# Kernel optimization log

Measured on AMD Instinct MI355X. Metric: run time of the kernel, lower is better.

Reference implementation:

```python
import jax, jax.numpy as jnp
import numpy as np

N = 50000   # nodes
E = 1600000 # edges
D = 128     # input_dim
H = 128     # hidden_dim
O = 128     # output_dim
G = 64      # graphs in batch
EPS = 1e-5  # batchnorm eps


def setup_inputs() -> dict:
    key = jax.random.key(0)
    ks = jax.random.split(key, 20)
    x = jax.random.normal(ks[0], (N, D), jnp.float32)
    edge_index = jax.random.randint(ks[1], (2, E), 0, N, dtype=jnp.int32)
    batch = jnp.sort(jax.random.randint(ks[2], (N,), 0, G, dtype=jnp.int32))

    def lin(k, fi, fo):
        return jax.random.normal(k, (fi, fo), jnp.float32) / np.float32(np.sqrt(fi))

    return {
        "x": x, "edge_index": edge_index, "batch": batch,
        "W1": lin(ks[3], D, H), "b1": jnp.zeros((H,), jnp.float32),
        "W2": lin(ks[4], H, H), "b2": jnp.zeros((H,), jnp.float32),
        "W3": lin(ks[5], H, O), "b3": jnp.zeros((O,), jnp.float32),
        "g1": 1.0 + 0.1 * jax.random.normal(ks[6], (H,), jnp.float32),
        "be1": 0.1 * jax.random.normal(ks[7], (H,), jnp.float32),
        "rm1": 0.1 * jax.random.normal(ks[8], (H,), jnp.float32),
        "rv1": 0.5 + jax.random.uniform(ks[9], (H,), jnp.float32),
        "g2": 1.0 + 0.1 * jax.random.normal(ks[10], (H,), jnp.float32),
        "be2": 0.1 * jax.random.normal(ks[11], (H,), jnp.float32),
        "rm2": 0.1 * jax.random.normal(ks[12], (H,), jnp.float32),
        "rv2": 0.5 + jax.random.uniform(ks[13], (H,), jnp.float32),
    }


def _gcn_layer(h, W, b, row, col, norm):
    # h: [N, Fin] -> [N, Fout]; GCN: A_hat @ (h W) + b with sym-normalized A_hat
    h = h @ W
    msg = h[row] * norm[:, None]                      # [E+N, Fout] gather
    out = jax.ops.segment_sum(msg, col, num_segments=N)
    return out + b


def _bn_eval(h, g, be, rm, rv):
    return (h - rm) * jax.lax.rsqrt(rv + EPS) * g + be


def reference(x, edge_index, batch, W1, b1, W2, b2, W3, b3,
              g1, be1, rm1, rv1, g2, be2, rm2, rv2):
    # add self loops (PyG GCNConv default)
    loop = jnp.arange(N, dtype=edge_index.dtype)
    row = jnp.concatenate([edge_index[0], loop])
    col = jnp.concatenate([edge_index[1], loop])
    deg = jax.ops.segment_sum(jnp.ones_like(col, jnp.float32), col, num_segments=N)
    dinv = jnp.where(deg > 0, jax.lax.rsqrt(jnp.maximum(deg, 1.0)), 0.0)
    norm = dinv[row] * dinv[col]                       # [E+N]

    h = _gcn_layer(x, W1, b1, row, col, norm)
    h = jax.nn.relu(_bn_eval(h, g1, be1, rm1, rv1))    # dropout is identity (eval)
    h = _gcn_layer(h, W2, b2, row, col, norm)
    h = jax.nn.relu(_bn_eval(h, g2, be2, rm2, rv2))
    h = _gcn_layer(h, W3, b3, row, col, norm)
    # global_add_pool by graph id
    return jax.ops.segment_sum(h, batch, num_segments=G)  # [G, O]
```

## Files before the change

kernel.cpp:

```cpp
#include <hip/hip_runtime.h>
#include <hip/hip_bf16.h>

#define NN 50000
#define NE 1600000
#define DIM 128
#define NG 64
#define EPSV 1e-5f
#define NCHUNK 49
#define UNROLL 8
#define RUN 4

typedef __attribute__((ext_vector_type(8))) __bf16 bf16x8;
typedef __attribute__((ext_vector_type(2))) __bf16 bf16x2;
typedef __attribute__((ext_vector_type(16))) float f32x16;


__global__ void count_kernel(const int* __restrict__ ecol, int* __restrict__ cnt) {
    int e = blockIdx.x * 256 + threadIdx.x;
    if (e < NE) atomicAdd(&cnt[ecol[e]], 1);
}

__global__ void scan_chunk(const int* __restrict__ cnt, int* __restrict__ excl,
                           int* __restrict__ csum) {
    __shared__ int lds[256];
    int t = threadIdx.x;
    int base = blockIdx.x * 1024 + t * 4;
    int v0 = (base + 0 < NN) ? cnt[base + 0] : 0;
    int v1 = (base + 1 < NN) ? cnt[base + 1] : 0;
    int v2 = (base + 2 < NN) ? cnt[base + 2] : 0;
    int v3 = (base + 3 < NN) ? cnt[base + 3] : 0;
    int s = v0 + v1 + v2 + v3;
    lds[t] = s;
    __syncthreads();
    for (int off = 1; off < 256; off <<= 1) {
        int x = (t >= off) ? lds[t - off] : 0;
        __syncthreads();
        lds[t] += x;
        __syncthreads();
    }
    int run = lds[t] - s;
    if (t == 255) csum[blockIdx.x] = lds[t];
    if (base + 0 < NN) excl[base + 0] = run; run += v0;
    if (base + 1 < NN) excl[base + 1] = run; run += v1;
    if (base + 2 < NN) excl[base + 2] = run; run += v2;
    if (base + 3 < NN) excl[base + 3] = run;
}

__global__ void scan_tail(const int* __restrict__ csum, int* __restrict__ coff, int nch) {
    int l = threadIdx.x;
    int v = (l < nch) ? csum[l] : 0;
    int s = v;
    for (int o = 1; o < 64; o <<= 1) {
        int x = __shfl_up(s, o);
        if (l >= o) s += x;
    }
    if (l < nch) coff[l] = s - v;
}

__global__ void fixup_kernel(int* __restrict__ row_ptr, const int* __restrict__ coff,
                             const int* __restrict__ cnt, float* __restrict__ dinv,
                             int* __restrict__ cursor) {
    int n = blockIdx.x * 256 + threadIdx.x;
    if (n < NN) {
        int rp = row_ptr[n] + coff[n >> 10];
        row_ptr[n] = rp;
        cursor[n] = rp;
        dinv[n] = rsqrtf((float)(cnt[n] + 1));
    }
    if (n == 0) row_ptr[NN] = NE;
}

__global__ void fill_kernel(const int* __restrict__ erow, const int* __restrict__ ecol,
                            const float* __restrict__ dinv, int* __restrict__ cursor,
                            int* __restrict__ esrc, float* __restrict__ enorm) {
    int e = blockIdx.x * 256 + threadIdx.x;
    if (e < NE) {
        int r = erow[e], c = ecol[e];
        int pos = atomicAdd(&cursor[c], 1);
        esrc[pos] = r;
        enorm[pos] = dinv[r] * dinv[c];
    }
}

__global__ void bn_prep_kernel(const float* __restrict__ b1, const float* __restrict__ g1,
                               const float* __restrict__ be1, const float* __restrict__ rm1,
                               const float* __restrict__ rv1,
                               const float* __restrict__ b2, const float* __restrict__ g2,
                               const float* __restrict__ be2, const float* __restrict__ rm2,
                               const float* __restrict__ rv2,
                               float* __restrict__ sc1, float* __restrict__ sh1,
                               float* __restrict__ sc2, float* __restrict__ sh2) {
    int c = threadIdx.x;
    if (c < DIM) {
        float s1 = g1[c] * rsqrtf(rv1[c] + EPSV);
        sc1[c] = s1;
        sh1[c] = (b1[c] - rm1[c]) * s1 + be1[c];
        float s2 = g2[c] * rsqrtf(rv2[c] + EPSV);
        sc2[c] = s2;
        sh2[c] = (b2[c] - rm2[c]) * s2 + be2[c];
    }
}


__device__ __forceinline__ bf16x8 load8(const float* p) {
    float4 lo = ((const float4*)p)[0], hi = ((const float4*)p)[1];
    bf16x8 a;
    a[0] = (__bf16)lo.x; a[1] = (__bf16)lo.y; a[2] = (__bf16)lo.z; a[3] = (__bf16)lo.w;
    a[4] = (__bf16)hi.x; a[5] = (__bf16)hi.y; a[6] = (__bf16)hi.z; a[7] = (__bf16)hi.w;
    return a;
}
__device__ __forceinline__ bf16x8 load8(const __bf16* p) {
    return *(const bf16x8*)p;
}

template <typename T>
__global__ void __launch_bounds__(256) matmul_kernel(const T* __restrict__ h,
                                                     const float* __restrict__ W,
                                                     __bf16* __restrict__ t) {
    const int wave = threadIdx.x >> 6;
    const int lane = threadIdx.x & 63;
    const int col = wave * 32 + (lane & 31);
    const int khalf = (lane >> 5) * 8;

    bf16x8 b[8];
#pragma unroll
    for (int kc = 0; kc < 8; kc++) {
#pragma unroll
        for (int j = 0; j < 8; j++) {
            b[kc][j] = (__bf16)W[(kc * 16 + khalf + j) * DIM + col];
        }
    }

    const int ntiles = (NN + 31) / 32;
    for (int tile = blockIdx.x; tile < ntiles; tile += gridDim.x) {
        const int arow = tile * 32 + (lane & 31);
        const int arow_c = (arow < NN) ? arow : (NN - 1);
        f32x16 acc = {};
#pragma unroll
        for (int kc = 0; kc < 8; kc++) {
            bf16x8 a = load8(h + (size_t)arow_c * DIM + kc * 16 + khalf);
            acc = __builtin_amdgcn_mfma_f32_32x32x16_bf16(a, b[kc], acc, 0, 0, 0);
        }
#pragma unroll
        for (int r = 0; r < 16; r++) {
            int orow = tile * 32 + (r & 3) + 8 * (r >> 2) + 4 * (lane >> 5);
            if (orow < NN) t[(size_t)orow * DIM + col] = (__bf16)acc[r];
        }
    }
}


__device__ __forceinline__ void gather_core(
    const unsigned int* __restrict__ t32, const int* __restrict__ esrc,
    const float* __restrict__ enorm, int beg, int end, int lane,
    float& ax, float& ay) {
    for (int e = beg; e < end; e += UNROLL) {
        int   s[UNROLL];
        float w[UNROLL];
        unsigned int u[UNROLL];
#pragma unroll
        for (int i = 0; i < UNROLL; i++) {
            const bool ok = (e + i) < end;
            const int  ee = ok ? (e + i) : beg;
            s[i] = esrc[ee];
            w[i] = ok ? enorm[ee] : 0.f;
        }
#pragma unroll
        for (int i = 0; i < UNROLL; i++) u[i] = t32[(size_t)s[i] * 64 + lane];
#pragma unroll
        for (int i = 0; i < UNROLL; i++) {
            ax = fmaf(__uint_as_float(u[i] << 16), w[i], ax);
            ay = fmaf(__uint_as_float(u[i] & 0xffff0000u), w[i], ay);
        }
    }
}

__global__ void __launch_bounds__(256) gather_bn_kernel(
    const unsigned int* __restrict__ t32, const int* __restrict__ row_ptr,
    const int* __restrict__ esrc, const float* __restrict__ enorm,
    const float* __restrict__ dinv, const float* __restrict__ scale,
    const float* __restrict__ shift, __bf16* __restrict__ out) {
    const int lane = threadIdx.x & 63;
    const int n = __builtin_amdgcn_readfirstlane(blockIdx.x * 4 + (threadIdx.x >> 6));
    if (n >= NN) return;
    float ax = 0.f, ay = 0.f;
    const int beg = row_ptr[n], end = row_ptr[n + 1];
    gather_core(t32, esrc, enorm, beg, end, lane, ax, ay);
    {
        float w = dinv[n]; w *= w;
        const unsigned int u = t32[(size_t)n * 64 + lane];
        ax = fmaf(__uint_as_float(u << 16), w, ax);
        ay = fmaf(__uint_as_float(u & 0xffff0000u), w, ay);
    }
    const int c0 = lane * 2, c1 = c0 + 1;
    ax = fmaxf(fmaf(ax, scale[c0], shift[c0]), 0.f);
    ay = fmaxf(fmaf(ay, scale[c1], shift[c1]), 0.f);
    bf16x2 o; o[0] = (__bf16)ax; o[1] = (__bf16)ay;
    *(bf16x2*)(out + (size_t)n * DIM + c0) = o;
}


__global__ void __launch_bounds__(256) gather_pool_kernel(
    const unsigned int* __restrict__ t32, const int* __restrict__ row_ptr,
    const int* __restrict__ esrc, const float* __restrict__ enorm,
    const float* __restrict__ dinv, const float* __restrict__ bias,
    const int* __restrict__ batch, float* __restrict__ out) {
    const int lane = threadIdx.x & 63;
    const int wid = __builtin_amdgcn_readfirstlane(blockIdx.x * 4 + (threadIdx.x >> 6));
    const int n0 = wid * RUN;
    if (n0 >= NN) return;
    const int n1 = (n0 + RUN < NN) ? n0 + RUN : NN;
    const int c0 = lane * 2, c1 = c0 + 1;
    const float bx = bias[c0], by = bias[c1];
    float rx = 0.f, ry = 0.f;
    int g = batch[n0];
    for (int n = n0; n < n1; ++n) {
        float ax = 0.f, ay = 0.f;
        const int beg = row_ptr[n], end = row_ptr[n + 1];
        gather_core(t32, esrc, enorm, beg, end, lane, ax, ay);
        {
            float w = dinv[n]; w *= w;
            const unsigned int u = t32[(size_t)n * 64 + lane];
            ax = fmaf(__uint_as_float(u << 16), w, ax);
            ay = fmaf(__uint_as_float(u & 0xffff0000u), w, ay);
        }
        const int gn = batch[n];
        if (gn != g) {
            atomicAdd(out + (size_t)g * DIM + c0, rx);
            atomicAdd(out + (size_t)g * DIM + c1, ry);
            rx = 0.f; ry = 0.f; g = gn;
        }
        rx += ax + bx;
        ry += ay + by;
    }
    atomicAdd(out + (size_t)g * DIM + c0, rx);
    atomicAdd(out + (size_t)g * DIM + c1, ry);
}


extern "C" void kernel_launch(void* const* d_in, const int* in_sizes, int n_in,
                              void* d_out, int out_size, void* d_ws, size_t ws_size,
                              hipStream_t stream) {
    const float* x    = (const float*)d_in[0];
    const int*   ei   = (const int*)d_in[1];
    const int*   batch= (const int*)d_in[2];
    const float* W1 = (const float*)d_in[3];
    const float* b1 = (const float*)d_in[4];
    const float* W2 = (const float*)d_in[5];
    const float* b2 = (const float*)d_in[6];
    const float* W3 = (const float*)d_in[7];
    const float* b3 = (const float*)d_in[8];
    const float* g1 = (const float*)d_in[9];
    const float* be1= (const float*)d_in[10];
    const float* rm1= (const float*)d_in[11];
    const float* rv1= (const float*)d_in[12];
    const float* g2 = (const float*)d_in[13];
    const float* be2= (const float*)d_in[14];
    const float* rm2= (const float*)d_in[15];
    const float* rv2= (const float*)d_in[16];
    const int* erow = ei;
    const int* ecol = ei + NE;

    char* ws = (char*)d_ws;
    size_t off = 0;
    auto alloc = [&](size_t bytes) -> void* {
        void* p = ws + off;
        off = (off + bytes + 255) & ~(size_t)255;
        return p;
    };
    int*    cnt     = (int*)alloc(NN * sizeof(int));
    int*    row_ptr = (int*)alloc((NN + 1) * sizeof(int));
    int*    cursor  = (int*)alloc(NN * sizeof(int));
    int*    csum    = (int*)alloc(64 * sizeof(int));
    int*    coff    = (int*)alloc(64 * sizeof(int));
    float*  dinv    = (float*)alloc(NN * sizeof(float));
    int*    esrc    = (int*)alloc(NE * sizeof(int));
    float*  enorm   = (float*)alloc(NE * sizeof(float));
    __bf16* tbuf    = (__bf16*)alloc((size_t)NN * DIM * sizeof(__bf16));
    __bf16* hbuf    = (__bf16*)alloc((size_t)NN * DIM * sizeof(__bf16));
    float*  sc1     = (float*)alloc(DIM * sizeof(float));
    float*  sh1     = (float*)alloc(DIM * sizeof(float));
    float*  sc2     = (float*)alloc(DIM * sizeof(float));
    float*  sh2     = (float*)alloc(DIM * sizeof(float));

    hipMemsetAsync(cnt, 0, NN * sizeof(int), stream);
    hipMemsetAsync(d_out, 0, NG * DIM * sizeof(float), stream);

    bn_prep_kernel<<<1, 128, 0, stream>>>(b1, g1, be1, rm1, rv1,
                                          b2, g2, be2, rm2, rv2,
                                          sc1, sh1, sc2, sh2);
    count_kernel<<<(NE + 255) / 256, 256, 0, stream>>>(ecol, cnt);
    scan_chunk<<<NCHUNK, 256, 0, stream>>>(cnt, row_ptr, csum);
    scan_tail<<<1, 64, 0, stream>>>(csum, coff, NCHUNK);
    fixup_kernel<<<(NN + 255) / 256, 256, 0, stream>>>(row_ptr, coff, cnt, dinv, cursor);
    fill_kernel<<<(NE + 255) / 256, 256, 0, stream>>>(erow, ecol, dinv, cursor, esrc, enorm);

    const unsigned int* t32 = (const unsigned int*)tbuf;
    const int nblk = (NN + 3) / 4;
    const int nwaves_pool = (NN + RUN - 1) / RUN;
    const int nblk_pool = (nwaves_pool + 3) / 4;

    matmul_kernel<float><<<512, 256, 0, stream>>>(x, W1, tbuf);
    gather_bn_kernel<<<nblk, 256, 0, stream>>>(t32, row_ptr, esrc, enorm, dinv,
                                               sc1, sh1, hbuf);
    matmul_kernel<__bf16><<<512, 256, 0, stream>>>(hbuf, W2, tbuf);
    gather_bn_kernel<<<nblk, 256, 0, stream>>>(t32, row_ptr, esrc, enorm, dinv,
                                               sc2, sh2, hbuf);
    matmul_kernel<__bf16><<<512, 256, 0, stream>>>(hbuf, W3, tbuf);
    gather_pool_kernel<<<nblk_pool, 256, 0, stream>>>(t32, row_ptr, esrc, enorm, dinv,
                                                      b3, batch, (float*)d_out);
}
```

Baseline: 457.0 us.

## Factor symmetric normalization into matmul epilogue and gather output, drop per-edge norm array

The per-edge weight dinv[r]*dinv[c] is split into two factors. The source-side dinv is applied to each row in the matmul epilogue, and the destination-side dinv is applied once per node after aggregation. This removes the enorm array entirely: it is no longer written in the fill kernel or read once per edge in each of the three gather passes, and the fill kernel stops doing random dinv lookups. The cost is an extra dinv load per output element in the matmul epilogue, plus rounding the pre-scaled values to bf16 at a different point.

```diff
diff --git a/kernel.cpp b/kernel.cpp
--- a/kernel.cpp
+++ b/kernel.cpp
@@ -71,14 +71,11 @@
 }
 
 __global__ void fill_kernel(const int* __restrict__ erow, const int* __restrict__ ecol,
-                            const float* __restrict__ dinv, int* __restrict__ cursor,
-                            int* __restrict__ esrc, float* __restrict__ enorm) {
+                            int* __restrict__ cursor, int* __restrict__ esrc) {
     int e = blockIdx.x * 256 + threadIdx.x;
     if (e < NE) {
-        int r = erow[e], c = ecol[e];
-        int pos = atomicAdd(&cursor[c], 1);
-        esrc[pos] = r;
-        enorm[pos] = dinv[r] * dinv[c];
+        int pos = atomicAdd(&cursor[ecol[e]], 1);
+        esrc[pos] = erow[e];
     }
 }
 
@@ -116,6 +113,7 @@
 template <typename T>
 __global__ void __launch_bounds__(256) matmul_kernel(const T* __restrict__ h,
                                                      const float* __restrict__ W,
+                                                     const float* __restrict__ dinv,
                                                      __bf16* __restrict__ t) {
     const int wave = threadIdx.x >> 6;
     const int lane = threadIdx.x & 63;
@@ -144,7 +142,7 @@
 #pragma unroll
         for (int r = 0; r < 16; r++) {
             int orow = tile * 32 + (r & 3) + 8 * (r >> 2) + 4 * (lane >> 5);
-            if (orow < NN) t[(size_t)orow * DIM + col] = (__bf16)acc[r];
+            if (orow < NN) t[(size_t)orow * DIM + col] = (__bf16)(acc[r] * dinv[orow]);
         }
     }
 }
@@ -152,8 +150,7 @@
 
 __device__ __forceinline__ void gather_core(
     const unsigned int* __restrict__ t32, const int* __restrict__ esrc,
-    const float* __restrict__ enorm, int beg, int end, int lane,
-    float& ax, float& ay) {
+    int beg, int end, int lane, float& ax, float& ay) {
     for (int e = beg; e < end; e += UNROLL) {
         int   s[UNROLL];
         float w[UNROLL];
@@ -161,9 +158,8 @@
 #pragma unroll
         for (int i = 0; i < UNROLL; i++) {
             const bool ok = (e + i) < end;
-            const int  ee = ok ? (e + i) : beg;
-            s[i] = esrc[ee];
-            w[i] = ok ? enorm[ee] : 0.f;
+            s[i] = esrc[ok ? (e + i) : beg];
+            w[i] = ok ? 1.f : 0.f;
         }
 #pragma unroll
         for (int i = 0; i < UNROLL; i++) u[i] = t32[(size_t)s[i] * 64 + lane];
@@ -177,24 +173,24 @@
 
 __global__ void __launch_bounds__(256) gather_bn_kernel(
     const unsigned int* __restrict__ t32, const int* __restrict__ row_ptr,
-    const int* __restrict__ esrc, const float* __restrict__ enorm,
-    const float* __restrict__ dinv, const float* __restrict__ scale,
-    const float* __restrict__ shift, __bf16* __restrict__ out) {
+    const int* __restrict__ esrc, const float* __restrict__ dinv,
+    const float* __restrict__ scale, const float* __restrict__ shift,
+    __bf16* __restrict__ out) {
     const int lane = threadIdx.x & 63;
     const int n = __builtin_amdgcn_readfirstlane(blockIdx.x * 4 + (threadIdx.x >> 6));
     if (n >= NN) return;
     float ax = 0.f, ay = 0.f;
     const int beg = row_ptr[n], end = row_ptr[n + 1];
-    gather_core(t32, esrc, enorm, beg, end, lane, ax, ay);
+    gather_core(t32, esrc, beg, end, lane, ax, ay);
     {
-        float w = dinv[n]; w *= w;
         const unsigned int u = t32[(size_t)n * 64 + lane];
-        ax = fmaf(__uint_as_float(u << 16), w, ax);
-        ay = fmaf(__uint_as_float(u & 0xffff0000u), w, ay);
-    }
+        ax += __uint_as_float(u << 16);
+        ay += __uint_as_float(u & 0xffff0000u);
+    }
+    const float dv = dinv[n];
     const int c0 = lane * 2, c1 = c0 + 1;
-    ax = fmaxf(fmaf(ax, scale[c0], shift[c0]), 0.f);
-    ay = fmaxf(fmaf(ay, scale[c1], shift[c1]), 0.f);
+    ax = fmaxf(fmaf(ax, dv * scale[c0], shift[c0]), 0.f);
+    ay = fmaxf(fmaf(ay, dv * scale[c1], shift[c1]), 0.f);
     bf16x2 o; o[0] = (__bf16)ax; o[1] = (__bf16)ay;
     *(bf16x2*)(out + (size_t)n * DIM + c0) = o;
 }
@@ -202,9 +198,9 @@
 
 __global__ void __launch_bounds__(256) gather_pool_kernel(
     const unsigned int* __restrict__ t32, const int* __restrict__ row_ptr,
-    const int* __restrict__ esrc, const float* __restrict__ enorm,
-    const float* __restrict__ dinv, const float* __restrict__ bias,
-    const int* __restrict__ batch, float* __restrict__ out) {
+    const int* __restrict__ esrc, const float* __restrict__ dinv,
+    const float* __restrict__ bias, const int* __restrict__ batch,
+    float* __restrict__ out) {
     const int lane = threadIdx.x & 63;
     const int wid = __builtin_amdgcn_readfirstlane(blockIdx.x * 4 + (threadIdx.x >> 6));
     const int n0 = wid * RUN;
@@ -217,21 +213,21 @@
     for (int n = n0; n < n1; ++n) {
         float ax = 0.f, ay = 0.f;
         const int beg = row_ptr[n], end = row_ptr[n + 1];
-        gather_core(t32, esrc, enorm, beg, end, lane, ax, ay);
+        gather_core(t32, esrc, beg, end, lane, ax, ay);
         {
-            float w = dinv[n]; w *= w;
             const unsigned int u = t32[(size_t)n * 64 + lane];
-            ax = fmaf(__uint_as_float(u << 16), w, ax);
-            ay = fmaf(__uint_as_float(u & 0xffff0000u), w, ay);
-        }
+            ax += __uint_as_float(u << 16);
+            ay += __uint_as_float(u & 0xffff0000u);
+        }
+        const float dv = dinv[n];
         const int gn = batch[n];
         if (gn != g) {
             atomicAdd(out + (size_t)g * DIM + c0, rx);
             atomicAdd(out + (size_t)g * DIM + c1, ry);
             rx = 0.f; ry = 0.f; g = gn;
         }
-        rx += ax + bx;
-        ry += ay + by;
+        rx += fmaf(ax, dv, bx);
+        ry += fmaf(ay, dv, by);
     }
     atomicAdd(out + (size_t)g * DIM + c0, rx);
     atomicAdd(out + (size_t)g * DIM + c1, ry);
@@ -275,7 +271,6 @@
     int*    coff    = (int*)alloc(64 * sizeof(int));
     float*  dinv    = (float*)alloc(NN * sizeof(float));
     int*    esrc    = (int*)alloc(NE * sizeof(int));
-    float*  enorm   = (float*)alloc(NE * sizeof(float));
     __bf16* tbuf    = (__bf16*)alloc((size_t)NN * DIM * sizeof(__bf16));
     __bf16* hbuf    = (__bf16*)alloc((size_t)NN * DIM * sizeof(__bf16));
     float*  sc1     = (float*)alloc(DIM * sizeof(float));
@@ -293,20 +288,20 @@
     scan_chunk<<<NCHUNK, 256, 0, stream>>>(cnt, row_ptr, csum);
     scan_tail<<<1, 64, 0, stream>>>(csum, coff, NCHUNK);
     fixup_kernel<<<(NN + 255) / 256, 256, 0, stream>>>(row_ptr, coff, cnt, dinv, cursor);
-    fill_kernel<<<(NE + 255) / 256, 256, 0, stream>>>(erow, ecol, dinv, cursor, esrc, enorm);
+    fill_kernel<<<(NE + 255) / 256, 256, 0, stream>>>(erow, ecol, cursor, esrc);
 
     const unsigned int* t32 = (const unsigned int*)tbuf;
     const int nblk = (NN + 3) / 4;
     const int nwaves_pool = (NN + RUN - 1) / RUN;
     const int nblk_pool = (nwaves_pool + 3) / 4;
 
-    matmul_kernel<float><<<512, 256, 0, stream>>>(x, W1, tbuf);
-    gather_bn_kernel<<<nblk, 256, 0, stream>>>(t32, row_ptr, esrc, enorm, dinv,
+    matmul_kernel<float><<<512, 256, 0, stream>>>(x, W1, dinv, tbuf);
+    gather_bn_kernel<<<nblk, 256, 0, stream>>>(t32, row_ptr, esrc, dinv,
                                                sc1, sh1, hbuf);
-    matmul_kernel<__bf16><<<512, 256, 0, stream>>>(hbuf, W2, tbuf);
-    gather_bn_kernel<<<nblk, 256, 0, stream>>>(t32, row_ptr, esrc, enorm, dinv,
+    matmul_kernel<__bf16><<<512, 256, 0, stream>>>(hbuf, W2, dinv, tbuf);
+    gather_bn_kernel<<<nblk, 256, 0, stream>>>(t32, row_ptr, esrc, dinv,
                                                sc2, sh2, hbuf);
-    matmul_kernel<__bf16><<<512, 256, 0, stream>>>(hbuf, W3, tbuf);
-    gather_pool_kernel<<<nblk_pool, 256, 0, stream>>>(t32, row_ptr, esrc, enorm, dinv,
+    matmul_kernel<__bf16><<<512, 256, 0, stream>>>(hbuf, W3, dinv, tbuf);
+    gather_pool_kernel<<<nblk_pool, 256, 0, stream>>>(t32, row_ptr, esrc, dinv,
                                                       b3, batch, (float*)d_out);
 }
```

After: 439.7 us. 3.8% less time.
